# Kernel optimization log

Hardware: AMD Instinct MI355X
Metric: run time of the kernel (lower is better)

The kernel has to match this reference:

```python
import jax, jax.numpy as jnp
import numpy as np

C_IN, D_STATE, EXPAND, KS = 64, 16, 2, 3
D_INNER = EXPAND * C_IN
HP_KS, HP_SIGMA = 15, 3.0
B, H, W = 4, 256, 256


def _gauss2d(ks, sigma):
    ax = jnp.arange(ks, dtype=jnp.float32) - (ks - 1) / 2.0
    g = jnp.exp(-(ax ** 2) / (2.0 * sigma ** 2))
    g = g / g.sum()
    return jnp.outer(g, g)


def _dwconv(x, w, pad):
    # x: [B,d,H,W], w: [d,1,kh,kw] depthwise
    return jax.lax.conv_general_dilated(
        x, w, window_strides=(1, 1), padding=[(pad, pad), (pad, pad)],
        dimension_numbers=("NCHW", "OIHW", "NCHW"),
        feature_group_count=x.shape[1])


def _selective_scan(u, dt, Bm, Cm, A, D, scan_axis):
    # u, dt: [B,d,H,W]; Bm, Cm: [B,N,H,W]; scan over scan_axis (2 or 3)
    u_s = jnp.moveaxis(u, scan_axis, 0)    # [L,B,d,M]
    dt_s = jnp.moveaxis(dt, scan_axis, 0)
    B_s = jnp.moveaxis(Bm, scan_axis, 0)   # [L,B,N,M]
    C_s = jnp.moveaxis(Cm, scan_axis, 0)
    Bb, d = u.shape[0], u.shape[1]
    M = u_s.shape[-1]
    N = A.shape[1]

    def step(h, inp):
        uj, dtj, Bj, Cj = inp                     # [B,d,M], [B,d,M], [B,N,M], [B,N,M]
        expA = jnp.exp(dtj[..., None] * A[None, :, None, :])   # [B,d,M,N]
        Bt = jnp.transpose(Bj, (0, 2, 1))[:, None]              # [B,1,M,N]
        Ct = jnp.transpose(Cj, (0, 2, 1))[:, None]
        h = expA * h + (uj * dtj)[..., None] * Bt               # [B,d,M,N]
        y = jnp.sum(h * Ct, axis=-1) + D[None, :, None] * uj    # [B,d,M]
        return h, y

    h0 = jnp.zeros((Bb, d, M, N), u.dtype)
    _, ys = jax.lax.scan(step, h0, (u_s, dt_s, B_s, C_s))
    return jnp.moveaxis(ys, 0, scan_axis)


def setup_inputs() -> dict:
    key = jax.random.key(0)
    ks = jax.random.split(key, 12)
    d, N = D_INNER, D_STATE
    A_log = -(jnp.linspace(0.0, 1.0, N, dtype=jnp.float32) * jnp.log(10.0))
    A_log = jnp.broadcast_to(A_log[None, :], (d, N)).astype(jnp.float32)
    return {
        "x": jax.random.normal(ks[0], (B, C_IN, H, W), jnp.float32),
        "in_proj_w": jax.random.normal(ks[1], (2 * d, C_IN), jnp.float32) * 0.05,
        "in_proj_b": jnp.zeros((2 * d,), jnp.float32),
        "dw_w": jax.random.normal(ks[2], (d, 1, KS, KS), jnp.float32) * 0.2,
        "dw_b": jnp.zeros((d,), jnp.float32),
        "xproj_w": jax.random.normal(ks[3], (1 + 2 * N, d), jnp.float32) * 0.05,
        "dtproj_w": jax.random.normal(ks[4], (d, 1), jnp.float32) * 0.5,
        "dtproj_b": jax.random.normal(ks[5], (d,), jnp.float32) * 0.5 - 4.0,
        "A_log": A_log,
        "D": jnp.ones((d,), jnp.float32),
        "out_w": jax.random.normal(ks[6], (C_IN, d), jnp.float32) * 0.05,
        "out_b": jnp.zeros((C_IN,), jnp.float32),
    }


def reference(x, in_proj_w, in_proj_b, dw_w, dw_b, xproj_w,
              dtproj_w, dtproj_b, A_log, D, out_w, out_b):
    d, N = D_INNER, D_STATE
    # in_proj (1x1 conv)
    uz = jnp.einsum("bchw,oc->bohw", x, in_proj_w) + in_proj_b[None, :, None, None]
    U, Z = uz[:, :d], uz[:, d:]
    # depthwise conv
    Uc = _dwconv(U, dw_w, KS // 2) + dw_b[None, :, None, None]
    # tanh(alpha * x) * weight + bias with alpha=0.5, weight=1, bias=0
    Uc = jnp.tanh(0.5 * Uc)
    # Gaussian high-pass: x - depthwise gaussian blur
    g = _gauss2d(HP_KS, HP_SIGMA)
    gk = jnp.broadcast_to(g[None, None], (d, 1, HP_KS, HP_KS))
    Uc = Uc - _dwconv(Uc, gk, HP_KS // 2)
    # x_proj (1x1 conv, no bias)
    params = jnp.einsum("bchw,oc->bohw", Uc, xproj_w)
    delta_in = params[:, :1]                 # [B,1,H,W]
    B_map = params[:, 1:1 + N]               # [B,N,H,W]
    C_map = params[:, 1 + N:1 + 2 * N]
    dt = jax.nn.softplus(jnp.einsum("bohw,do->bdhw", delta_in, dtproj_w)
                         + dtproj_b[None, :, None, None])
    A = -jnp.exp(A_log)
    Y_h = _selective_scan(Uc, dt, B_map, C_map, A, D, scan_axis=3)   # scan over W
    Y_v = _selective_scan(Y_h, dt, B_map, C_map, A, D, scan_axis=2)  # scan over H
    out = Y_v * jax.nn.sigmoid(Z)
    return jnp.einsum("bdhw,cd->bchw", out, out_w) + out_b[None, :, None, None]
```

## Files before the change

kernel.cpp:

```cpp
#include <hip/hip_runtime.h>
#include <hip/hip_bf16.h>
#include <math.h>

#define BB 4
#define CIN 64
#define DI 128
#define NS 16
#define HH 256
#define WW 256
#define HW 65536
#define NCH_P 33

__device__ __forceinline__ float softplusf(float x) {
    return fmaxf(x, 0.f) + __logf(1.0f + __expf(-fabsf(x)));
}
__device__ __forceinline__ float tanh_half(float a) {
    return 1.0f - 2.0f / (1.0f + __expf(a));
}
__device__ __forceinline__ float sigmoidf(float z) {
    return 1.0f / (1.0f + __expf(-z));
}

__device__ __forceinline__ void gauss15(float* g) {
    float s = 0.f;
#pragma unroll
    for (int i = 0; i < 15; ++i) {
        float a = (float)i - 7.0f;
        g[i] = __expf(-a * a / 18.0f);
        s += g[i];
    }
    float inv = 1.0f / s;
#pragma unroll
    for (int i = 0; i < 15; ++i) g[i] *= inv;
}

__global__ __launch_bounds__(256) void k_inproj(
    const float* __restrict__ xb, const float* __restrict__ w,
    const float* __restrict__ bias, float* __restrict__ Ub) {
    int p = blockIdx.x * 256 + threadIdx.x;
    int og = blockIdx.y * 64;
    float xv[CIN];
#pragma unroll
    for (int c = 0; c < CIN; ++c) xv[c] = xb[(size_t)c * HW + p];
#pragma unroll 2
    for (int o = og; o < og + 64; ++o) {
        float a0 = bias[o], a1 = 0.f, a2 = 0.f, a3 = 0.f;
        const float* wr = w + o * CIN;
#pragma unroll
        for (int c = 0; c < CIN; c += 4) {
            a0 = fmaf(xv[c],     wr[c],     a0);
            a1 = fmaf(xv[c + 1], wr[c + 1], a1);
            a2 = fmaf(xv[c + 2], wr[c + 2], a2);
            a3 = fmaf(xv[c + 3], wr[c + 3], a3);
        }
        Ub[(size_t)o * HW + p] = (a0 + a1) + (a2 + a3);
    }
}

#define TILE_H 16
__global__ __launch_bounds__(256) void k_conv(
    const float* __restrict__ Ub, const float* __restrict__ dww,
    const float* __restrict__ dwb, float* __restrict__ Ucb) {
    __shared__ float sU[32 * 256];
    __shared__ float sC[30 * 272];
    int c  = blockIdx.x >> 4;
    int t  = blockIdx.x & 15;
    int h0 = t * TILE_H;
    int w  = threadIdx.x;

    const float* base = Ub + (size_t)c * HW;
#pragma unroll
    for (int i = 0; i < 32; ++i) {
        int hh = h0 + i - 8;
        sU[i * 256 + w] = (hh >= 0 && hh < HH) ? base[hh * WW + w] : 0.f;
    }
    __syncthreads();

    float wt[9];
#pragma unroll
    for (int i = 0; i < 9; ++i) wt[i] = dww[c * 9 + i];
    float bb = dwb[c];

#pragma unroll
    for (int i = 0; i < 30; ++i) {
        int r = h0 + i - 7;
        float v = 0.f;
        if (r >= 0 && r < HH) {
            float acc = bb;
#pragma unroll
            for (int ky = 0; ky < 3; ++ky) {
                const float* ur = sU + (i + ky) * 256;
#pragma unroll
                for (int kx = 0; kx < 3; ++kx) {
                    int ww = w + kx - 1;
                    if (ww >= 0 && ww < WW) acc = fmaf(ur[ww], wt[ky * 3 + kx], acc);
                }
            }
            v = tanh_half(acc);
        }
        sC[i * 272 + w + 7] = v;
    }
    if (w < 7) {
#pragma unroll
        for (int i = 0; i < 30; ++i) { sC[i * 272 + w] = 0.f; sC[i * 272 + w + 263] = 0.f; }
    }
    __syncthreads();

    float g[15]; gauss15(g);
#pragma unroll
    for (int i = 0; i < 30; ++i) {
        float acc = 0.f;
#pragma unroll
        for (int k = 0; k < 15; ++k) acc = fmaf(sC[i * 272 + w + k], g[k], acc);
        sU[i * 256 + w] = acc;
    }
    float* outp = Ucb + (size_t)c * HW + h0 * WW + w;
#pragma unroll
    for (int i = 0; i < TILE_H; ++i) {
        float acc = 0.f;
#pragma unroll
        for (int k = 0; k < 15; ++k) acc = fmaf(sU[(i + k) * 256 + w], g[k], acc);
        float center = sC[(i + 7) * 272 + w + 7];
        outp[i * WW] = center - acc;
    }
}

__global__ __launch_bounds__(256) void k_xproj(
    const float* __restrict__ Uc, const float* __restrict__ xw,
    float* __restrict__ P) {
    int p = blockIdx.x * 256 + threadIdx.x;
    int b = p >> 16;
    int rem = p & 65535;
    const float* up = Uc + (size_t)b * DI * HW + rem;
    float acc[NCH_P];
#pragma unroll
    for (int o = 0; o < NCH_P; ++o) acc[o] = 0.f;
    for (int c = 0; c < DI; ++c) {
        float u = up[(size_t)c * HW];
#pragma unroll
        for (int o = 0; o < NCH_P; ++o) acc[o] = fmaf(u, xw[o * DI + c], acc[o]);
    }
    float* pp = P + (size_t)b * NCH_P * HW + rem;
#pragma unroll
    for (int o = 0; o < NCH_P; ++o) pp[(size_t)o * HW] = acc[o];
}

#define CW 32
__global__ __launch_bounds__(128) void k_scan_w(
    float* __restrict__ UY, const float* __restrict__ P,
    const float* __restrict__ A_log, const float* __restrict__ dtw,
    const float* __restrict__ dtb, const float* __restrict__ Dv) {
    __shared__ float sU[DI * 33];
    __shared__ float sP[CW * 36];
    int bh = blockIdx.x;
    int b = bh >> 8;
    int h = bh & 255;
    int t = threadIdx.x;

    float Av[NS];
#pragma unroll
    for (int n = 0; n < NS; ++n) Av[n] = -__expf(A_log[t * NS + n]);
    float wdt = dtw[t], bdt = dtb[t], Dd = Dv[t];
    float hS[NS];
#pragma unroll
    for (int n = 0; n < NS; ++n) hS[n] = 0.f;

    float* ubase = UY + (size_t)(b * DI) * HW + (size_t)h * WW;
    const float* prow = P + (size_t)(b * NCH_P) * HW + (size_t)h * WW;

    const int w4 = (t & 7) * 4;
    const int dbase = t >> 3;

    float4 rU[8];
    float rP[9];
#pragma unroll
    for (int p = 0; p < 8; ++p)
        rU[p] = *(const float4*)(ubase + (size_t)(dbase + p * 16) * HW + w4);
#pragma unroll
    for (int i = 0; i < 9; ++i) {
        int idx = i * 128 + t, ch = idx >> 5, wi = idx & 31;
        rP[i] = (ch < NCH_P) ? prow[(size_t)ch * HW + wi] : 0.f;
    }

    for (int w0 = 0; w0 < WW; w0 += CW) {
#pragma unroll
        for (int p = 0; p < 8; ++p) {
            float* s = sU + (dbase + p * 16) * 33 + w4;
            s[0] = rU[p].x; s[1] = rU[p].y; s[2] = rU[p].z; s[3] = rU[p].w;
        }
#pragma unroll
        for (int i = 0; i < 9; ++i) {
            int idx = i * 128 + t, ch = idx >> 5, wi = idx & 31;
            if (ch < NCH_P) sP[wi * 36 + ch] = rP[i];
        }
        __syncthreads();
        if (w0 + CW < WW) {
#pragma unroll
            for (int p = 0; p < 8; ++p)
                rU[p] = *(const float4*)(ubase + (size_t)(dbase + p * 16) * HW + w0 + CW + w4);
#pragma unroll
            for (int i = 0; i < 9; ++i) {
                int idx = i * 128 + t, ch = idx >> 5, wi = idx & 31;
                rP[i] = (ch < NCH_P) ? prow[(size_t)ch * HW + w0 + CW + wi] : 0.f;
            }
        }
#pragma unroll 2
        for (int wi = 0; wi < CW; ++wi) {
            const float* pr = sP + wi * 36;
            float4 q0 = *(const float4*)(pr);
            float4 q1 = *(const float4*)(pr + 4);
            float4 q2 = *(const float4*)(pr + 8);
            float4 q3 = *(const float4*)(pr + 12);
            float4 q4 = *(const float4*)(pr + 16);
            float4 q5 = *(const float4*)(pr + 20);
            float4 q6 = *(const float4*)(pr + 24);
            float4 q7 = *(const float4*)(pr + 28);
            float q8 = pr[32];
            float u = sU[t * 33 + wi];
            float dt = softplusf(fmaf(q0.x, wdt, bdt));
            float ud = u * dt;
            float y = Dd * u;
            float Bv[NS] = {q0.y,q0.z,q0.w,q1.x,q1.y,q1.z,q1.w,q2.x,
                            q2.y,q2.z,q2.w,q3.x,q3.y,q3.z,q3.w,q4.x};
            float Cv[NS] = {q4.y,q4.z,q4.w,q5.x,q5.y,q5.z,q5.w,q6.x,
                            q6.y,q6.z,q6.w,q7.x,q7.y,q7.z,q7.w,q8};
#pragma unroll
            for (int n = 0; n < NS; ++n) {
                float e = __expf(dt * Av[n]);
                hS[n] = fmaf(e, hS[n], ud * Bv[n]);
                y = fmaf(hS[n], Cv[n], y);
            }
            sU[t * 33 + wi] = y;
        }
        __syncthreads();
#pragma unroll
        for (int p = 0; p < 8; ++p) {
            const float* s = sU + (dbase + p * 16) * 33 + w4;
            float4 v; v.x = s[0]; v.y = s[1]; v.z = s[2]; v.w = s[3];
            *(float4*)(ubase + (size_t)(dbase + p * 16) * HW + w0 + w4) = v;
        }
        __syncthreads();
    }
}

__global__ __launch_bounds__(256) void k_scan_h(
    float* __restrict__ UY, const float* __restrict__ P,
    const float* __restrict__ A_log, const float* __restrict__ dtw,
    const float* __restrict__ dtb, const float* __restrict__ Dv) {
    int bd = blockIdx.x;
    int b = bd >> 7;
    int d = bd & (DI - 1);
    int w = threadIdx.x;
    float Av[NS];
#pragma unroll
    for (int n = 0; n < NS; ++n) Av[n] = -__expf(A_log[d * NS + n]);
    float wdt = dtw[d], bdt = dtb[d], Dd = Dv[d];
    float* ucol = UY + (size_t)bd * HW + w;
    const float* pcol = P + (size_t)(b * NCH_P) * HW + w;
    float hS[NS];
#pragma unroll
    for (int n = 0; n < NS; ++n) hS[n] = 0.f;

    float uA, deA, BA[NS], CA[NS];
    float uB, deB, Bb[NS], Cb[NS];
    uA = ucol[0]; deA = pcol[0];
#pragma unroll
    for (int n = 0; n < NS; ++n) { BA[n] = pcol[(size_t)(1 + n) * HW]; CA[n] = pcol[(size_t)(17 + n) * HW]; }
    uB = ucol[WW]; deB = pcol[WW];
#pragma unroll
    for (int n = 0; n < NS; ++n) { Bb[n] = pcol[(size_t)(1 + n) * HW + WW]; Cb[n] = pcol[(size_t)(17 + n) * HW + WW]; }

    for (int h = 0; h < HH; h += 2) {
        size_t o2 = (size_t)min(h + 2, HH - 1) * WW;
        size_t o3 = (size_t)min(h + 3, HH - 1) * WW;
        float u2 = ucol[o2], de2 = pcol[o2];
        float u3 = ucol[o3], de3 = pcol[o3];
        float B2[NS], C2[NS], B3[NS], C3[NS];
#pragma unroll
        for (int n = 0; n < NS; ++n) {
            B2[n] = pcol[(size_t)(1 + n) * HW + o2];
            C2[n] = pcol[(size_t)(17 + n) * HW + o2];
            B3[n] = pcol[(size_t)(1 + n) * HW + o3];
            C3[n] = pcol[(size_t)(17 + n) * HW + o3];
        }
        {
            float dt = softplusf(fmaf(deA, wdt, bdt));
            float ud = uA * dt;
            float y = Dd * uA;
#pragma unroll
            for (int n = 0; n < NS; ++n) {
                float e = __expf(dt * Av[n]);
                hS[n] = fmaf(e, hS[n], ud * BA[n]);
                y = fmaf(hS[n], CA[n], y);
            }
            ucol[(size_t)h * WW] = y;
        }
        {
            float dt = softplusf(fmaf(deB, wdt, bdt));
            float ud = uB * dt;
            float y = Dd * uB;
#pragma unroll
            for (int n = 0; n < NS; ++n) {
                float e = __expf(dt * Av[n]);
                hS[n] = fmaf(e, hS[n], ud * Bb[n]);
                y = fmaf(hS[n], Cb[n], y);
            }
            ucol[(size_t)(h + 1) * WW] = y;
        }
        uA = u2; deA = de2; uB = u3; deB = de3;
#pragma unroll
        for (int n = 0; n < NS; ++n) { BA[n] = B2[n]; CA[n] = C2[n]; Bb[n] = B3[n]; Cb[n] = C3[n]; }
    }
}

__global__ __launch_bounds__(256) void k_gate(
    float* __restrict__ Y, const float* __restrict__ x,
    const float* __restrict__ wz, const float* __restrict__ bz) {
    int p = blockIdx.x * 256 + threadIdx.x;
    int b = p >> 16;
    int rem = p & 65535;
    const float* xp = x + (size_t)b * CIN * HW + rem;
    float xv[CIN];
#pragma unroll
    for (int c = 0; c < CIN; ++c) xv[c] = xp[(size_t)c * HW];
    float* yp = Y + (size_t)b * DI * HW + rem;
#pragma unroll 2
    for (int dd = 0; dd < DI; ++dd) {
        float z0 = 0.f, z1 = 0.f, z2 = 0.f, z3 = 0.f;
        const float* wr = wz + dd * CIN;
#pragma unroll
        for (int c = 0; c < CIN; c += 4) {
            z0 = fmaf(xv[c],     wr[c],     z0);
            z1 = fmaf(xv[c + 1], wr[c + 1], z1);
            z2 = fmaf(xv[c + 2], wr[c + 2], z2);
            z3 = fmaf(xv[c + 3], wr[c + 3], z3);
        }
        float z = bz[dd] + ((z0 + z1) + (z2 + z3));
        float yv = yp[(size_t)dd * HW];
        yp[(size_t)dd * HW] = yv * sigmoidf(z);
    }
}

__global__ __launch_bounds__(256) void k_out2(
    const float* __restrict__ G, const float* __restrict__ ow,
    const float* __restrict__ ob, float* __restrict__ outp) {
    int p = blockIdx.x * 256 + threadIdx.x;
    int b = p >> 16;
    int rem = p & 65535;
    const float* gp = G + (size_t)b * DI * HW + rem;
    float acc[CIN];
#pragma unroll
    for (int c = 0; c < CIN; ++c) acc[c] = 0.f;
    for (int dd = 0; dd < DI; ++dd) {
        float g = gp[(size_t)dd * HW];
#pragma unroll
        for (int c = 0; c < CIN; ++c) acc[c] = fmaf(g, ow[c * DI + dd], acc[c]);
    }
    float* op = outp + (size_t)b * CIN * HW + rem;
#pragma unroll
    for (int c = 0; c < CIN; ++c) op[(size_t)c * HW] = acc[c] + ob[c];
}

extern "C" void kernel_launch(void* const* d_in, const int* in_sizes, int n_in,
                              void* d_out, int out_size, void* d_ws, size_t ws_size,
                              hipStream_t stream) {
    const float* x     = (const float*)d_in[0];
    const float* ipw   = (const float*)d_in[1];
    const float* ipb   = (const float*)d_in[2];
    const float* dww   = (const float*)d_in[3];
    const float* dwb   = (const float*)d_in[4];
    const float* xpw   = (const float*)d_in[5];
    const float* dtw   = (const float*)d_in[6];
    const float* dtb   = (const float*)d_in[7];
    const float* A_log = (const float*)d_in[8];
    const float* Dv    = (const float*)d_in[9];
    const float* ow    = (const float*)d_in[10];
    const float* ob    = (const float*)d_in[11];
    float* out = (float*)d_out;

    const float* wz = ipw + (size_t)DI * CIN;
    const float* bz = ipb + DI;

    const size_t PLANE = (size_t)DI * HW;
    const size_t NB    = (size_t)BB * PLANE;

    if (ws_size >= (NB + PLANE) * sizeof(float)) {
        float* bufY = (float*)d_ws;
        float* bufU = bufY + NB;
        float* P    = out;
        for (int b = 0; b < BB; ++b) {
            k_inproj<<<dim3(HW / 256, 2), 256, 0, stream>>>(x + (size_t)b * CIN * HW, ipw, ipb, bufU);
            k_conv<<<DI * 16, 256, 0, stream>>>(bufU, dww, dwb, bufY + (size_t)b * PLANE);
        }
        k_xproj<<<BB * (HW / 256), 256, 0, stream>>>(bufY, xpw, P);
        k_scan_w<<<BB * HH, 128, 0, stream>>>(bufY, P, A_log, dtw, dtb, Dv);
        k_scan_h<<<BB * DI, 256, 0, stream>>>(bufY, P, A_log, dtw, dtb, Dv);
        k_gate<<<BB * (HW / 256), 256, 0, stream>>>(bufY, x, wz, bz);
        k_out2<<<BB * (HW / 256), 256, 0, stream>>>(bufY, ow, ob, out);
    } else {
        float* bufA = (float*)d_ws;
        float* bufY = bufA + PLANE;
        for (int b = 0; b < BB; ++b) {
            const float* xb = x + (size_t)b * CIN * HW;
            k_inproj<<<dim3(HW / 256, 2), 256, 0, stream>>>(xb, ipw, ipb, bufA);
            k_conv<<<DI * 16, 256, 0, stream>>>(bufA, dww, dwb, bufY);
            k_xproj<<<HW / 256, 256, 0, stream>>>(bufY, xpw, bufA);
            k_scan_w<<<HH, 128, 0, stream>>>(bufY, bufA, A_log, dtw, dtb, Dv);
            k_scan_h<<<DI, 256, 0, stream>>>(bufY, bufA, A_log, dtw, dtb, Dv);
            k_gate<<<HW / 256, 256, 0, stream>>>(bufY, xb, wz, bz);
            k_out2<<<HW / 256, 256, 0, stream>>>(bufY, ow, ob, out + (size_t)b * CIN * HW);
        }
    }
}
```

Before: 1.550 ms.

## Fuse gate into output projection, deepen scan_h prefetch, use 32-bit indexing

Merges the sigmoid gate and the output 1x1 projection into a single kernel, so the gated intermediate is never written back to global memory and reread. The vertical scan now prefetches four rows ahead in a register ring instead of two, with an occupancy hint of two blocks per CU. Per-plane address arithmetic switches from size_t to int offsets to cut 64-bit index math. The fused kernel holds many registers (64 accumulators plus 64 inputs), which may limit occupancy or cause spills.

```diff
diff --git a/kernel.cpp b/kernel.cpp
--- a/kernel.cpp
+++ b/kernel.cpp
@@ -41,7 +41,7 @@
     int og = blockIdx.y * 64;
     float xv[CIN];
 #pragma unroll
-    for (int c = 0; c < CIN; ++c) xv[c] = xb[(size_t)c * HW + p];
+    for (int c = 0; c < CIN; ++c) xv[c] = xb[c * HW + p];
 #pragma unroll 2
     for (int o = og; o < og + 64; ++o) {
         float a0 = bias[o], a1 = 0.f, a2 = 0.f, a3 = 0.f;
@@ -53,7 +53,7 @@
             a2 = fmaf(xv[c + 2], wr[c + 2], a2);
             a3 = fmaf(xv[c + 3], wr[c + 3], a3);
         }
-        Ub[(size_t)o * HW + p] = (a0 + a1) + (a2 + a3);
+        Ub[o * HW + p] = (a0 + a1) + (a2 + a3);
     }
 }
 
@@ -128,21 +128,21 @@
 __global__ __launch_bounds__(256) void k_xproj(
     const float* __restrict__ Uc, const float* __restrict__ xw,
     float* __restrict__ P) {
-    int p = blockIdx.x * 256 + threadIdx.x;
-    int b = p >> 16;
-    int rem = p & 65535;
-    const float* up = Uc + (size_t)b * DI * HW + rem;
+    int bp = blockIdx.x << 8;
+    int b = bp >> 16;
+    int rem = (bp & 65535) | threadIdx.x;
+    const float* ub_ = Uc + (size_t)b * DI * HW;
     float acc[NCH_P];
 #pragma unroll
     for (int o = 0; o < NCH_P; ++o) acc[o] = 0.f;
     for (int c = 0; c < DI; ++c) {
-        float u = up[(size_t)c * HW];
+        float u = ub_[c * HW + rem];
 #pragma unroll
         for (int o = 0; o < NCH_P; ++o) acc[o] = fmaf(u, xw[o * DI + c], acc[o]);
     }
-    float* pp = P + (size_t)b * NCH_P * HW + rem;
-#pragma unroll
-    for (int o = 0; o < NCH_P; ++o) pp[(size_t)o * HW] = acc[o];
+    float* pb_ = P + (size_t)b * NCH_P * HW;
+#pragma unroll
+    for (int o = 0; o < NCH_P; ++o) pb_[o * HW + rem] = acc[o];
 }
 
 #define CW 32
@@ -175,11 +175,11 @@
     float rP[9];
 #pragma unroll
     for (int p = 0; p < 8; ++p)
-        rU[p] = *(const float4*)(ubase + (size_t)(dbase + p * 16) * HW + w4);
+        rU[p] = *(const float4*)(ubase + ((dbase + p * 16) * HW + w4));
 #pragma unroll
     for (int i = 0; i < 9; ++i) {
         int idx = i * 128 + t, ch = idx >> 5, wi = idx & 31;
-        rP[i] = (ch < NCH_P) ? prow[(size_t)ch * HW + wi] : 0.f;
+        rP[i] = (ch < NCH_P) ? prow[ch * HW + wi] : 0.f;
     }
 
     for (int w0 = 0; w0 < WW; w0 += CW) {
@@ -197,11 +197,11 @@
         if (w0 + CW < WW) {
 #pragma unroll
             for (int p = 0; p < 8; ++p)
-                rU[p] = *(const float4*)(ubase + (size_t)(dbase + p * 16) * HW + w0 + CW + w4);
+                rU[p] = *(const float4*)(ubase + ((dbase + p * 16) * HW + w0 + CW + w4));
 #pragma unroll
             for (int i = 0; i < 9; ++i) {
                 int idx = i * 128 + t, ch = idx >> 5, wi = idx & 31;
-                rP[i] = (ch < NCH_P) ? prow[(size_t)ch * HW + w0 + CW + wi] : 0.f;
+                rP[i] = (ch < NCH_P) ? prow[ch * HW + w0 + CW + wi] : 0.f;
             }
         }
 #pragma unroll 2
@@ -237,13 +237,14 @@
         for (int p = 0; p < 8; ++p) {
             const float* s = sU + (dbase + p * 16) * 33 + w4;
             float4 v; v.x = s[0]; v.y = s[1]; v.z = s[2]; v.w = s[3];
-            *(float4*)(ubase + (size_t)(dbase + p * 16) * HW + w0 + w4) = v;
+            *(float4*)(ubase + ((dbase + p * 16) * HW + w0 + w4)) = v;
         }
         __syncthreads();
     }
 }
 
-__global__ __launch_bounds__(256) void k_scan_h(
+#define UNR 4
+__global__ __launch_bounds__(256, 2) void k_scan_h(
     float* __restrict__ UY, const float* __restrict__ P,
     const float* __restrict__ A_log, const float* __restrict__ dtw,
     const float* __restrict__ dtb, const float* __restrict__ Dv) {
@@ -255,79 +256,72 @@
 #pragma unroll
     for (int n = 0; n < NS; ++n) Av[n] = -__expf(A_log[d * NS + n]);
     float wdt = dtw[d], bdt = dtb[d], Dd = Dv[d];
-    float* ucol = UY + (size_t)bd * HW + w;
-    const float* pcol = P + (size_t)(b * NCH_P) * HW + w;
+    float* ub = UY + (size_t)bd * HW;
+    const float* pb = P + (size_t)b * NCH_P * HW;
     float hS[NS];
 #pragma unroll
     for (int n = 0; n < NS; ++n) hS[n] = 0.f;
 
-    float uA, deA, BA[NS], CA[NS];
-    float uB, deB, Bb[NS], Cb[NS];
-    uA = ucol[0]; deA = pcol[0];
-#pragma unroll
-    for (int n = 0; n < NS; ++n) { BA[n] = pcol[(size_t)(1 + n) * HW]; CA[n] = pcol[(size_t)(17 + n) * HW]; }
-    uB = ucol[WW]; deB = pcol[WW];
-#pragma unroll
-    for (int n = 0; n < NS; ++n) { Bb[n] = pcol[(size_t)(1 + n) * HW + WW]; Cb[n] = pcol[(size_t)(17 + n) * HW + WW]; }
-
-    for (int h = 0; h < HH; h += 2) {
-        size_t o2 = (size_t)min(h + 2, HH - 1) * WW;
-        size_t o3 = (size_t)min(h + 3, HH - 1) * WW;
-        float u2 = ucol[o2], de2 = pcol[o2];
-        float u3 = ucol[o3], de3 = pcol[o3];
-        float B2[NS], C2[NS], B3[NS], C3[NS];
+    float uf[UNR], df[UNR], Bf[UNR][NS], Cf[UNR][NS];
+#pragma unroll
+    for (int s = 0; s < UNR; ++s) {
+        int off = s * WW + w;
+        uf[s] = ub[off];
+        df[s] = pb[off];
 #pragma unroll
         for (int n = 0; n < NS; ++n) {
-            B2[n] = pcol[(size_t)(1 + n) * HW + o2];
-            C2[n] = pcol[(size_t)(17 + n) * HW + o2];
-            B3[n] = pcol[(size_t)(1 + n) * HW + o3];
-            C3[n] = pcol[(size_t)(17 + n) * HW + o3];
-        }
-        {
-            float dt = softplusf(fmaf(deA, wdt, bdt));
-            float ud = uA * dt;
-            float y = Dd * uA;
+            Bf[s][n] = pb[(1 + n) * HW + off];
+            Cf[s][n] = pb[(17 + n) * HW + off];
+        }
+    }
+
+    for (int h = 0; h < HH; h += UNR) {
+#pragma unroll
+        for (int s = 0; s < UNR; ++s) {
+            float u = uf[s], de = df[s];
+            float dt = softplusf(fmaf(de, wdt, bdt));
+            float ud = u * dt;
+            float y = Dd * u;
 #pragma unroll
             for (int n = 0; n < NS; ++n) {
                 float e = __expf(dt * Av[n]);
-                hS[n] = fmaf(e, hS[n], ud * BA[n]);
-                y = fmaf(hS[n], CA[n], y);
-            }
-            ucol[(size_t)h * WW] = y;
-        }
-        {
-            float dt = softplusf(fmaf(deB, wdt, bdt));
-            float ud = uB * dt;
-            float y = Dd * uB;
+                hS[n] = fmaf(e, hS[n], ud * Bf[s][n]);
+                y = fmaf(hS[n], Cf[s][n], y);
+            }
+            ub[(h + s) * WW + w] = y;
+            int hp = h + UNR + s; if (hp > HH - 1) hp = HH - 1;
+            int off = hp * WW + w;
+            uf[s] = ub[off];
+            df[s] = pb[off];
 #pragma unroll
             for (int n = 0; n < NS; ++n) {
-                float e = __expf(dt * Av[n]);
-                hS[n] = fmaf(e, hS[n], ud * Bb[n]);
-                y = fmaf(hS[n], Cb[n], y);
-            }
-            ucol[(size_t)(h + 1) * WW] = y;
-        }
-        uA = u2; deA = de2; uB = u3; deB = de3;
-#pragma unroll
-        for (int n = 0; n < NS; ++n) { BA[n] = B2[n]; CA[n] = C2[n]; Bb[n] = B3[n]; Cb[n] = C3[n]; }
-    }
-}
-
-__global__ __launch_bounds__(256) void k_gate(
-    float* __restrict__ Y, const float* __restrict__ x,
-    const float* __restrict__ wz, const float* __restrict__ bz) {
-    int p = blockIdx.x * 256 + threadIdx.x;
-    int b = p >> 16;
-    int rem = p & 65535;
-    const float* xp = x + (size_t)b * CIN * HW + rem;
+                Bf[s][n] = pb[(1 + n) * HW + off];
+                Cf[s][n] = pb[(17 + n) * HW + off];
+            }
+        }
+    }
+}
+
+__global__ __launch_bounds__(256, 2) void k_gateout(
+    const float* __restrict__ Y, const float* __restrict__ x,
+    const float* __restrict__ wz, const float* __restrict__ bz,
+    const float* __restrict__ ow, const float* __restrict__ ob,
+    float* __restrict__ outp) {
+    int bp = blockIdx.x << 8;
+    int b = bp >> 16;
+    int rem = (bp & 65535) | threadIdx.x;
+    const float* xb = x + (size_t)b * CIN * HW;
+    const float* yb = Y + (size_t)b * DI * HW;
     float xv[CIN];
 #pragma unroll
-    for (int c = 0; c < CIN; ++c) xv[c] = xp[(size_t)c * HW];
-    float* yp = Y + (size_t)b * DI * HW + rem;
+    for (int c = 0; c < CIN; ++c) xv[c] = xb[c * HW + rem];
+    float acc[CIN];
+#pragma unroll
+    for (int c = 0; c < CIN; ++c) acc[c] = 0.f;
 #pragma unroll 2
     for (int dd = 0; dd < DI; ++dd) {
+        const float* wr = wz + dd * CIN;
         float z0 = 0.f, z1 = 0.f, z2 = 0.f, z3 = 0.f;
-        const float* wr = wz + dd * CIN;
 #pragma unroll
         for (int c = 0; c < CIN; c += 4) {
             z0 = fmaf(xv[c],     wr[c],     z0);
@@ -336,29 +330,13 @@
             z3 = fmaf(xv[c + 3], wr[c + 3], z3);
         }
         float z = bz[dd] + ((z0 + z1) + (z2 + z3));
-        float yv = yp[(size_t)dd * HW];
-        yp[(size_t)dd * HW] = yv * sigmoidf(z);
-    }
-}
-
-__global__ __launch_bounds__(256) void k_out2(
-    const float* __restrict__ G, const float* __restrict__ ow,
-    const float* __restrict__ ob, float* __restrict__ outp) {
-    int p = blockIdx.x * 256 + threadIdx.x;
-    int b = p >> 16;
-    int rem = p & 65535;
-    const float* gp = G + (size_t)b * DI * HW + rem;
-    float acc[CIN];
-#pragma unroll
-    for (int c = 0; c < CIN; ++c) acc[c] = 0.f;
-    for (int dd = 0; dd < DI; ++dd) {
-        float g = gp[(size_t)dd * HW];
+        float g = yb[dd * HW + rem] * sigmoidf(z);
 #pragma unroll
         for (int c = 0; c < CIN; ++c) acc[c] = fmaf(g, ow[c * DI + dd], acc[c]);
     }
-    float* op = outp + (size_t)b * CIN * HW + rem;
-#pragma unroll
-    for (int c = 0; c < CIN; ++c) op[(size_t)c * HW] = acc[c] + ob[c];
+    float* op = outp + (size_t)b * CIN * HW;
+#pragma unroll
+    for (int c = 0; c < CIN; ++c) op[c * HW + rem] = acc[c] + ob[c];
 }
 
 extern "C" void kernel_launch(void* const* d_in, const int* in_sizes, int n_in,
@@ -395,8 +373,7 @@
         k_xproj<<<BB * (HW / 256), 256, 0, stream>>>(bufY, xpw, P);
         k_scan_w<<<BB * HH, 128, 0, stream>>>(bufY, P, A_log, dtw, dtb, Dv);
         k_scan_h<<<BB * DI, 256, 0, stream>>>(bufY, P, A_log, dtw, dtb, Dv);
-        k_gate<<<BB * (HW / 256), 256, 0, stream>>>(bufY, x, wz, bz);
-        k_out2<<<BB * (HW / 256), 256, 0, stream>>>(bufY, ow, ob, out);
+        k_gateout<<<BB * (HW / 256), 256, 0, stream>>>(bufY, x, wz, bz, ow, ob, out);
     } else {
         float* bufA = (float*)d_ws;
         float* bufY = bufA + PLANE;
@@ -407,8 +384,7 @@
             k_xproj<<<HW / 256, 256, 0, stream>>>(bufY, xpw, bufA);
             k_scan_w<<<HH, 128, 0, stream>>>(bufY, bufA, A_log, dtw, dtb, Dv);
             k_scan_h<<<DI, 256, 0, stream>>>(bufY, bufA, A_log, dtw, dtb, Dv);
-            k_gate<<<HW / 256, 256, 0, stream>>>(bufY, xb, wz, bz);
-            k_out2<<<HW / 256, 256, 0, stream>>>(bufY, ow, ob, out + (size_t)b * CIN * HW);
-        }
-    }
-}
+            k_gateout<<<HW / 256, 256, 0, stream>>>(bufY, xb, wz, bz, ow, ob, out + (size_t)b * CIN * HW);
+        }
+    }
+}
```

Measured after the change: 2.990 ms. 1.93x slower.
